# Performance work log

Hardware: AMD Instinct MI355X
Metric: run time of the kernel (lower is better)

## Reference

```python
import jax, jax.numpy as jnp
import numpy as np
import math

B, T, C = 2, 2048, 1024
H = 16            # n_head
RATIO = 4         # ratio_kv
HKV = H // RATIO  # n_head_kv = 4
HD = C // H       # head_dim = 64
G = H // HKV      # query heads per kv head = 4


def _alibi_slopes(n_heads):
    # n_heads must be a power of 2 here (H=16)
    assert math.log2(n_heads).is_integer()
    start = 2.0 ** (-(2.0 ** (-(math.log2(n_heads) - 3))))
    return np.array([start * (start ** i) for i in range(n_heads)], dtype=np.float32)


def setup_inputs() -> dict:
    key = jax.random.key(0)
    ks = jax.random.split(key, 5)
    return {
        "x": jax.random.normal(ks[0], (B, T, C), dtype=jnp.float32),
        "Wq": jax.random.normal(ks[1], (C, C), dtype=jnp.float32) * 0.02,
        "Wk": jax.random.normal(ks[2], (C, HKV * HD), dtype=jnp.float32) * 0.02,
        "Wv": jax.random.normal(ks[3], (C, HKV * HD), dtype=jnp.float32) * 0.02,
        "Wo": jax.random.normal(ks[4], (C, C), dtype=jnp.float32) * 0.02,
    }


def reference(x, Wq, Wk, Wv, Wo):
    # GQA causal attention with ALiBi bias (flash-disabled fallback path).
    # q: [B,HKV,G,T,HD] (grouped query heads), k/v: [B,HKV,T,HD]
    q = (x @ Wq).reshape(B, T, H, HD).transpose(0, 2, 1, 3).reshape(B, HKV, G, T, HD)
    k = (x @ Wk).reshape(B, T, HKV, HD).transpose(0, 2, 1, 3)
    v = (x @ Wv).reshape(B, T, HKV, HD).transpose(0, 2, 1, 3)

    scale = 1.0 / math.sqrt(HD)
    att = jnp.einsum('bkgtd,bksd->bkgts', q, k) * scale  # [B,HKV,G,T,T]

    # ALiBi: original repeats alibi(n_head) by G and truncates to n_head,
    # so query head h uses slope get_slopes(H)[h // G] == slopes[:HKV] per kv group.
    slopes = jnp.asarray(_alibi_slopes(H))[:HKV]          # [HKV]
    pos = jnp.arange(T)
    rel = (pos[None, :] - pos[:, None]).astype(jnp.float32)  # [T,T], rel[i,j]=j-i
    bias = slopes[:, None, None] * rel                    # [HKV,T,T]
    causal = jnp.triu(jnp.full((T, T), -jnp.inf, dtype=jnp.float32), 1)

    att = att + bias[None, :, None] + causal
    att = jax.nn.softmax(att.astype(jnp.float32), axis=-1).astype(q.dtype)

    y = jnp.einsum('bkgts,bksd->bkgtd', att, v)           # [B,HKV,G,T,HD]
    y = y.reshape(B, H, T, HD).transpose(0, 2, 1, 3).reshape(B, T, C)
    return y @ Wo
```

## Files before the change

kernel.cpp:

```cpp
#include <hip/hip_runtime.h>
#include <hip/hip_bf16.h>
#include <math.h>

#define B_ 2
#define T_ 2048
#define C_ 1024
#define H_ 16
#define HKV_ 4
#define G_ 4
#define HD_ 64
#define KVC_ 256
#define NQKV_ 1536
#define NQT_ 32

typedef __attribute__((ext_vector_type(8))) short bf16x8;
typedef __attribute__((ext_vector_type(4))) float f32x4;

static __device__ inline short f2bf(float f) {
    __hip_bfloat16 h = __float2bfloat16(f);
    short s;
    __builtin_memcpy(&s, &h, 2);
    return s;
}
static __device__ inline float bf2f(short s) {
    unsigned int u = ((unsigned int)(unsigned short)s) << 16;
    float f;
    __builtin_memcpy(&f, &u, 4);
    return f;
}

static __device__ inline void gload_lds16(const short* g, short* lds) {
    __builtin_amdgcn_global_load_lds(
        (const __attribute__((address_space(1))) unsigned int*)g,
        (__attribute__((address_space(3))) unsigned int*)lds, 16, 0, 0);
}

template <int CTRL>
static __device__ inline float dpp_mov(float x) {
    int xi = __builtin_bit_cast(int, x);
    int r = __builtin_amdgcn_update_dpp(0, xi, CTRL, 0xF, 0xF, true);
    return __builtin_bit_cast(float, r);
}
static __device__ inline float dpp_sum16(float x) {
    x += dpp_mov<0xB1>(x);
    x += dpp_mov<0x4E>(x);
    x += dpp_mov<0x141>(x);
    x += dpp_mov<0x140>(x);
    return x;
}

__global__ __launch_bounds__(256) void cast_bf16(
    const float* __restrict__ in, short* __restrict__ out, int n)
{
    const int i = (blockIdx.x * 256 + threadIdx.x) * 8;
    if (i >= n) return;
    const float4 a = *(const float4*)(in + i);
    const float4 b = *(const float4*)(in + i + 4);
    bf16x8 o;
    o[0] = f2bf(a.x); o[1] = f2bf(a.y); o[2] = f2bf(a.z); o[3] = f2bf(a.w);
    o[4] = f2bf(b.x); o[5] = f2bf(b.y); o[6] = f2bf(b.z); o[7] = f2bf(b.w);
    *(bf16x8*)(out + i) = o;
}

__global__ __launch_bounds__(256) void w_transpose(
    const float* __restrict__ Wq, const float* __restrict__ Wk,
    const float* __restrict__ Wv, const float* __restrict__ Wo,
    short* __restrict__ Wt, short* __restrict__ Wot)
{
    const int z = blockIdx.z;
    const float* in;
    short* out;
    int N;
    if (z == 0)      { in = Wq; out = Wt;                     N = C_; }
    else if (z == 1) { in = Wk; out = Wt + C_ * C_;           N = KVC_; }
    else if (z == 2) { in = Wv; out = Wt + (C_ + KVC_) * C_;  N = KVC_; }
    else             { in = Wo; out = Wot;                    N = C_; }
    const int n0 = blockIdx.x * 32;
    if (n0 >= N) return;
    __shared__ float t[32][33];
    const int tx = threadIdx.x, ty = threadIdx.y;
    const int k0 = blockIdx.y * 32;
    #pragma unroll
    for (int j = 0; j < 4; j++)
        t[ty + j * 8][tx] = in[(size_t)(k0 + ty + j * 8) * N + n0 + tx];
    __syncthreads();
    #pragma unroll
    for (int j = 0; j < 4; j++)
        out[(size_t)(n0 + ty + j * 8) * C_ + k0 + tx] = f2bf(t[tx][ty + j * 8]);
}

template <bool OUT_BF16>
__global__ __launch_bounds__(256) void gemm_bf16(
    const short* __restrict__ A, const short* __restrict__ Bt,
    void* __restrict__ Cout, int M, int N, int K)
{
    __shared__ short As[64 * 32];
    __shared__ short Bs[128 * 32];
    const int tid = threadIdx.x;
    const int wave = tid >> 6, lane = tid & 63;
    const int l15 = lane & 15, quad = lane >> 4;
    const int row0 = blockIdx.y * 64, col0 = blockIdx.x * 128;
    const int wrow = (wave >> 1) * 32, wcol = (wave & 1) * 64;

    f32x4 acc[2][4];
    #pragma unroll
    for (int i = 0; i < 2; i++)
        #pragma unroll
        for (int j = 0; j < 4; j++)
            acc[i][j] = (f32x4){0.f, 0.f, 0.f, 0.f};

    for (int kt = 0; kt < K; kt += 32) {
        __syncthreads();
        {
            const int r = wave * 16 + (lane >> 2);
            const int kof = (lane & 3) * 8;
            gload_lds16(A + (size_t)(row0 + r) * K + kt + kof, &As[wave * 512]);
        }
        #pragma unroll
        for (int c2 = 0; c2 < 2; c2++) {
            const int c = wave * 2 + c2;
            const int r = c * 16 + (lane >> 2);
            const int kof = (lane & 3) * 8;
            gload_lds16(Bt + (size_t)(col0 + r) * K + kt + kof, &Bs[c * 512]);
        }
        __syncthreads();

        bf16x8 af[2], bf[4];
        #pragma unroll
        for (int mt = 0; mt < 2; mt++)
            af[mt] = *(const bf16x8*)&As[(wrow + mt * 16 + l15) * 32 + quad * 8];
        #pragma unroll
        for (int nt = 0; nt < 4; nt++)
            bf[nt] = *(const bf16x8*)&Bs[(wcol + nt * 16 + l15) * 32 + quad * 8];
        #pragma unroll
        for (int mt = 0; mt < 2; mt++)
            #pragma unroll
            for (int nt = 0; nt < 4; nt++)
                acc[mt][nt] = __builtin_amdgcn_mfma_f32_16x16x32_bf16(
                    af[mt], bf[nt], acc[mt][nt], 0, 0, 0);
    }

    #pragma unroll
    for (int mt = 0; mt < 2; mt++) {
        #pragma unroll
        for (int r = 0; r < 4; r++) {
            const size_t row = row0 + wrow + mt * 16 + quad * 4 + r;
            #pragma unroll
            for (int nt = 0; nt < 4; nt++) {
                const size_t col = col0 + wcol + nt * 16 + l15;
                if (OUT_BF16)
                    ((short*)Cout)[row * N + col] = f2bf(acc[mt][nt][r]);
                else
                    ((float*)Cout)[row * N + col] = acc[mt][nt][r];
            }
        }
    }
}

__global__ __launch_bounds__(256) void kv_tile(
    const short* __restrict__ QKV, short* __restrict__ Kt, short* __restrict__ Vt)
{
    __shared__ short Ls[64 * 72];
    const int jt = blockIdx.x;
    const int bk = blockIdx.y;
    const int b = bk >> 2, kh = bk & 3;
    const int tid = threadIdx.x;
    const int key = tid >> 2, d16 = (tid & 3) * 16;
    const size_t src = (size_t)(b * T_ + jt * 64 + key) * NQKV_ + C_ + kh * 64 + d16;
    const size_t tbase = (size_t)(bk * 32 + jt) * 4096;

    {
        const int db0 = (tid & 3) * 2, db1 = db0 + 1;
        *(bf16x8*)(Kt + tbase + key * 64 + ((db0 ^ (key & 7)) * 8)) =
            *(const bf16x8*)(QKV + src);
        *(bf16x8*)(Kt + tbase + key * 64 + ((db1 ^ (key & 7)) * 8)) =
            *(const bf16x8*)(QKV + src + 8);
    }
    *(bf16x8*)&Ls[key * 72 + d16]     = *(const bf16x8*)(QKV + src + KVC_);
    *(bf16x8*)&Ls[key * 72 + d16 + 8] = *(const bf16x8*)(QKV + src + KVC_ + 8);
    __syncthreads();
    const int d = tid >> 2, k16 = (tid & 3) * 16;
    bf16x8 o0, o1;
    #pragma unroll
    for (int i = 0; i < 8; i++) o0[i] = Ls[(k16 + i) * 72 + d];
    #pragma unroll
    for (int i = 0; i < 8; i++) o1[i] = Ls[(k16 + 8 + i) * 72 + d];
    const int kb0 = (tid & 3) * 2, kb1 = kb0 + 1;
    *(bf16x8*)(Vt + tbase + d * 64 + ((kb0 ^ (d & 7)) * 8)) = o0;
    *(bf16x8*)(Vt + tbase + d * 64 + ((kb1 ^ (d & 7)) * 8)) = o1;
}

#define LSTR 72

__global__ __launch_bounds__(256) void attn_mfma(
    const short* __restrict__ QKV, const short* __restrict__ Ktg,
    const short* __restrict__ Vtg, short* __restrict__ Y)
{
    const int qx = blockIdx.x;
    const int bh = blockIdx.y;
    const int qtL = qx, qtH = NQT_ - 1 - qx;
    const int b = bh >> 4, h = bh & 15, kh = h >> 2;
    const float slope = exp2f(-0.5f * (float)(kh + 1));
    const int tid = threadIdx.x;
    const int wave = tid >> 6, lane = tid & 63;
    const int l15 = lane & 15, quad = lane >> 4;
    const int lswz = (l15 & 7) * 8;

    __shared__ short Ks[4096];
    __shared__ short Vs[4096];
    __shared__ short Ps[4 * 32 * LSTR];
    short* Pw = &Ps[wave * 32 * LSTR];
    const int wswz = ((quad >> 1) & 1) << 4;
    const int rswz = ((l15 >> 3) & 1) << 4;

    const size_t bT = (size_t)b * T_;
    const size_t tb0 = (size_t)((b * HKV_ + kh) * 32) * 4096;
    const int qrow0H = qtH * 64 + wave * 16;
    const int qrow0L = qtL * 64 + wave * 16;

    bf16x8 qfH[2], qfL[2];
    #pragma unroll
    for (int k0 = 0; k0 < 2; k0++) {
        const short* qpH = QKV + (bT + qrow0H + l15) * NQKV_ + h * 64;
        const short* qpL = QKV + (bT + qrow0L + l15) * NQKV_ + h * 64;
        bf16x8 rH = *(const bf16x8*)(qpH + k0 * 32 + quad * 8);
        bf16x8 rL = *(const bf16x8*)(qpL + k0 * 32 + quad * 8);
        #pragma unroll
        for (int j = 0; j < 8; j++) {
            qfH[k0][j] = f2bf(bf2f(rH[j]) * 0.125f);
            qfL[k0][j] = f2bf(bf2f(rL[j]) * 0.125f);
        }
    }

    f32x4 OaccH[4], OaccL[4];
    float psumH[4], psumL[4];
    #pragma unroll
    for (int nt = 0; nt < 4; nt++) {
        OaccH[nt] = (f32x4){0.f, 0.f, 0.f, 0.f};
        OaccL[nt] = (f32x4){0.f, 0.f, 0.f, 0.f};
    }
    #pragma unroll
    for (int r = 0; r < 4; r++) { psumH[r] = 0.f; psumL[r] = 0.f; }

    for (int jtk = 0; jtk <= qtH; jtk++) {
        __syncthreads();
        {
            const short* Ktile = Ktg + tb0 + (size_t)jtk * 4096;
            const short* Vtile = Vtg + tb0 + (size_t)jtk * 4096;
            #pragma unroll
            for (int i = 0; i < 2; i++) {
                const int ch = wave * 2 + i;
                gload_lds16(Ktile + ch * 512 + lane * 8, &Ks[ch * 512]);
                gload_lds16(Vtile + ch * 512 + lane * 8, &Vs[ch * 512]);
            }
        }
        __syncthreads();

        const bool doL = (jtk <= qtL);

        bf16x8 kf[8];
        #pragma unroll
        for (int nt = 0; nt < 4; nt++)
            #pragma unroll
            for (int k0 = 0; k0 < 2; k0++)
                kf[nt * 2 + k0] = *(const bf16x8*)
                    &Ks[(nt * 16 + l15) * 64 + (((k0 * 4 + quad) * 8) ^ lswz)];

        f32x4 sH[4], sL[4];
        #pragma unroll
        for (int nt = 0; nt < 4; nt++) {
            f32x4 a = {0.f, 0.f, 0.f, 0.f};
            a = __builtin_amdgcn_mfma_f32_16x16x32_bf16(qfH[0], kf[nt*2+0], a, 0, 0, 0);
            a = __builtin_amdgcn_mfma_f32_16x16x32_bf16(qfH[1], kf[nt*2+1], a, 0, 0, 0);
            sH[nt] = a;
        }
        if (doL) {
            #pragma unroll
            for (int nt = 0; nt < 4; nt++) {
                f32x4 a = {0.f, 0.f, 0.f, 0.f};
                a = __builtin_amdgcn_mfma_f32_16x16x32_bf16(qfL[0], kf[nt*2+0], a, 0, 0, 0);
                a = __builtin_amdgcn_mfma_f32_16x16x32_bf16(qfL[1], kf[nt*2+1], a, 0, 0, 0);
                sL[nt] = a;
            }
        }

        {
            const float relfH = (float)(jtk * 64 + l15 - quad * 4 - qrow0H);
            const bool mH = (jtk == qtH);
            #pragma unroll
            for (int nt = 0; nt < 4; nt++) {
                const int colsw = ((nt * 16 + l15) ^ wswz);
                #pragma unroll
                for (int r = 0; r < 4; r++) {
                    const float relv = relfH + (float)(nt * 16 - r);
                    float p = __expf(fmaf(slope, relv, sH[nt][r]));
                    if (mH && relv > 0.f) p = 0.f;
                    psumH[r] += p;
                    Pw[(quad * 4 + r) * LSTR + colsw] = f2bf(p);
                }
            }
        }
        if (doL) {
            const float relfL = (float)(jtk * 64 + l15 - quad * 4 - qrow0L);
            const bool mL = (jtk == qtL);
            #pragma unroll
            for (int nt = 0; nt < 4; nt++) {
                const int colsw = ((nt * 16 + l15) ^ wswz);
                #pragma unroll
                for (int r = 0; r < 4; r++) {
                    const float relv = relfL + (float)(nt * 16 - r);
                    float p = __expf(fmaf(slope, relv, sL[nt][r]));
                    if (mL && relv > 0.f) p = 0.f;
                    psumL[r] += p;
                    Pw[(16 + quad * 4 + r) * LSTR + colsw] = f2bf(p);
                }
            }
        }
        __asm__ volatile("s_waitcnt lgkmcnt(0)" ::: "memory");

        bf16x8 vf[8];
        #pragma unroll
        for (int nt = 0; nt < 4; nt++)
            #pragma unroll
            for (int k0 = 0; k0 < 2; k0++)
                vf[nt * 2 + k0] = *(const bf16x8*)
                    &Vs[(nt * 16 + l15) * 64 + (((k0 * 4 + quad) * 8) ^ lswz)];

        {
            bf16x8 pf0 = *(const bf16x8*)&Pw[l15 * LSTR + ((quad * 8) ^ rswz)];
            bf16x8 pf1 = *(const bf16x8*)&Pw[l15 * LSTR + ((32 + quad * 8) ^ rswz)];
            #pragma unroll
            for (int nt = 0; nt < 4; nt++) {
                OaccH[nt] = __builtin_amdgcn_mfma_f32_16x16x32_bf16(
                    pf0, vf[nt*2+0], OaccH[nt], 0, 0, 0);
                OaccH[nt] = __builtin_amdgcn_mfma_f32_16x16x32_bf16(
                    pf1, vf[nt*2+1], OaccH[nt], 0, 0, 0);
            }
        }
        if (doL) {
            bf16x8 pf0 = *(const bf16x8*)&Pw[(16 + l15) * LSTR + ((quad * 8) ^ rswz)];
            bf16x8 pf1 = *(const bf16x8*)&Pw[(16 + l15) * LSTR + ((32 + quad * 8) ^ rswz)];
            #pragma unroll
            for (int nt = 0; nt < 4; nt++) {
                OaccL[nt] = __builtin_amdgcn_mfma_f32_16x16x32_bf16(
                    pf0, vf[nt*2+0], OaccL[nt], 0, 0, 0);
                OaccL[nt] = __builtin_amdgcn_mfma_f32_16x16x32_bf16(
                    pf1, vf[nt*2+1], OaccL[nt], 0, 0, 0);
            }
        }
    }

    #pragma unroll
    for (int r = 0; r < 4; r++) {
        const float invH = 1.f / dpp_sum16(psumH[r]);
        const float invL = 1.f / dpp_sum16(psumL[r]);
        const int rowH = qrow0H + quad * 4 + r;
        const int rowL = qrow0L + quad * 4 + r;
        short* ypH = Y + (bT + rowH) * C_ + h * 64 + l15;
        short* ypL = Y + (bT + rowL) * C_ + h * 64 + l15;
        #pragma unroll
        for (int nt = 0; nt < 4; nt++) {
            ypH[nt * 16] = f2bf(OaccH[nt][r] * invH);
            ypL[nt * 16] = f2bf(OaccL[nt][r] * invL);
        }
    }
}

extern "C" void kernel_launch(void* const* d_in, const int* in_sizes, int n_in,
                              void* d_out, int out_size, void* d_ws, size_t ws_size,
                              hipStream_t stream) {
    const float* x  = (const float*)d_in[0];
    const float* Wq = (const float*)d_in[1];
    const float* Wk = (const float*)d_in[2];
    const float* Wv = (const float*)d_in[3];
    const float* Wo = (const float*)d_in[4];
    float* out = (float*)d_out;

    const int M = B_ * T_;
    short* xb  = (short*)d_ws;
    short* Wt  = xb  + (size_t)M * C_;
    short* Wot = Wt  + (size_t)NQKV_ * C_;
    short* QKV = Wot + (size_t)C_ * C_;
    short* Yb  = QKV + (size_t)M * NQKV_;
    short* Ktg = Yb  + (size_t)M * C_;
    short* Vtg = Ktg + (size_t)8 * 32 * 4096;

    cast_bf16<<<dim3(M * C_ / (256 * 8)), dim3(256), 0, stream>>>(x, xb, M * C_);
    w_transpose<<<dim3(32, 32, 4), dim3(32, 8), 0, stream>>>(Wq, Wk, Wv, Wo, Wt, Wot);

    gemm_bf16<true><<<dim3(NQKV_ / 128, M / 64), dim3(256), 0, stream>>>(
        xb, Wt, QKV, M, NQKV_, C_);
    kv_tile<<<dim3(32, 8), dim3(256), 0, stream>>>(QKV, Ktg, Vtg);
    attn_mfma<<<dim3(NQT_ / 2, B_ * H_), dim3(256), 0, stream>>>(QKV, Ktg, Vtg, Yb);
    gemm_bf16<false><<<dim3(C_ / 128, M / 64), dim3(256), 0, stream>>>(
        Yb, Wot, out, M, C_, C_);
}
```

Before: 182.2 us.

## Compute softmax row sums via MFMA with ones and use exp2 with truncated bf16

Folds log2(e) into the query scale and ALiBi slope so the exponent becomes a raw exp2, and splits the diagonal tile from the others so only the last tile pays for the causal mask check. The per-lane psum accumulation and final DPP reduction are replaced by extra MFMAs of P against a ones vector, so the row sums come from the same bf16 P values used for P·V. P is converted to bf16 by truncation instead of rounding, which makes the VALU-heavy softmax section cheaper. In exchange it adds two MFMAs per tile per half and introduces a slight downward bias in P from truncation.

```diff
diff --git a/kernel.cpp b/kernel.cpp
--- a/kernel.cpp
+++ b/kernel.cpp
@@ -22,6 +22,11 @@
     __builtin_memcpy(&s, &h, 2);
     return s;
 }
+static __device__ inline short f2bf_trunc(float f) {
+    unsigned int u;
+    __builtin_memcpy(&u, &f, 4);
+    return (short)(u >> 16);
+}
 static __device__ inline float bf2f(short s) {
     unsigned int u = ((unsigned int)(unsigned short)s) << 16;
     float f;
@@ -33,20 +38,6 @@
     __builtin_amdgcn_global_load_lds(
         (const __attribute__((address_space(1))) unsigned int*)g,
         (__attribute__((address_space(3))) unsigned int*)lds, 16, 0, 0);
-}
-
-template <int CTRL>
-static __device__ inline float dpp_mov(float x) {
-    int xi = __builtin_bit_cast(int, x);
-    int r = __builtin_amdgcn_update_dpp(0, xi, CTRL, 0xF, 0xF, true);
-    return __builtin_bit_cast(float, r);
-}
-static __device__ inline float dpp_sum16(float x) {
-    x += dpp_mov<0xB1>(x);
-    x += dpp_mov<0x4E>(x);
-    x += dpp_mov<0x141>(x);
-    x += dpp_mov<0x140>(x);
-    return x;
 }
 
 __global__ __launch_bounds__(256) void cast_bf16(
@@ -200,7 +191,7 @@
     const int bh = blockIdx.y;
     const int qtL = qx, qtH = NQT_ - 1 - qx;
     const int b = bh >> 4, h = bh & 15, kh = h >> 2;
-    const float slope = exp2f(-0.5f * (float)(kh + 1));
+    const float slope2 = exp2f(-0.5f * (float)(kh + 1)) * 1.44269504f;
     const int tid = threadIdx.x;
     const int wave = tid >> 6, lane = tid & 63;
     const int l15 = lane & 15, quad = lane >> 4;
@@ -218,6 +209,7 @@
     const int qrow0H = qtH * 64 + wave * 16;
     const int qrow0L = qtL * 64 + wave * 16;
 
+    const float qscale = 0.125f * 1.44269504f;
     bf16x8 qfH[2], qfL[2];
     #pragma unroll
     for (int k0 = 0; k0 < 2; k0++) {
@@ -227,20 +219,22 @@
         bf16x8 rL = *(const bf16x8*)(qpL + k0 * 32 + quad * 8);
         #pragma unroll
         for (int j = 0; j < 8; j++) {
-            qfH[k0][j] = f2bf(bf2f(rH[j]) * 0.125f);
-            qfL[k0][j] = f2bf(bf2f(rL[j]) * 0.125f);
-        }
-    }
-
-    f32x4 OaccH[4], OaccL[4];
-    float psumH[4], psumL[4];
+            qfH[k0][j] = f2bf(bf2f(rH[j]) * qscale);
+            qfL[k0][j] = f2bf(bf2f(rL[j]) * qscale);
+        }
+    }
+
+    const short one_s = (short)0x3F80;
+    const bf16x8 ones = {one_s, one_s, one_s, one_s, one_s, one_s, one_s, one_s};
+
+    f32x4 OaccH[4], OaccL[4], laccH, laccL;
     #pragma unroll
     for (int nt = 0; nt < 4; nt++) {
         OaccH[nt] = (f32x4){0.f, 0.f, 0.f, 0.f};
         OaccL[nt] = (f32x4){0.f, 0.f, 0.f, 0.f};
     }
-    #pragma unroll
-    for (int r = 0; r < 4; r++) { psumH[r] = 0.f; psumL[r] = 0.f; }
+    laccH = (f32x4){0.f, 0.f, 0.f, 0.f};
+    laccL = (f32x4){0.f, 0.f, 0.f, 0.f};
 
     for (int jtk = 0; jtk <= qtH; jtk++) {
         __syncthreads();
@@ -285,34 +279,60 @@
         }
 
         {
-            const float relfH = (float)(jtk * 64 + l15 - quad * 4 - qrow0H);
-            const bool mH = (jtk == qtH);
-            #pragma unroll
-            for (int nt = 0; nt < 4; nt++) {
-                const int colsw = ((nt * 16 + l15) ^ wswz);
+            const float base = slope2 * (float)(jtk * 64 + l15 - quad * 4 - qrow0H);
+            if (jtk == qtH) {
                 #pragma unroll
-                for (int r = 0; r < 4; r++) {
-                    const float relv = relfH + (float)(nt * 16 - r);
-                    float p = __expf(fmaf(slope, relv, sH[nt][r]));
-                    if (mH && relv > 0.f) p = 0.f;
-                    psumH[r] += p;
-                    Pw[(quad * 4 + r) * LSTR + colsw] = f2bf(p);
+                for (int nt = 0; nt < 4; nt++) {
+                    const int colsw = ((nt * 16 + l15) ^ wswz);
+                    #pragma unroll
+                    for (int r = 0; r < 4; r++) {
+                        const float relv = (float)(jtk * 64 + l15 - quad * 4 - qrow0H)
+                                         + (float)(nt * 16 - r);
+                        float p = __builtin_amdgcn_exp2f(
+                            fmaf(slope2, (float)(nt * 16 - r), base) + sH[nt][r]);
+                        if (relv > 0.f) p = 0.f;
+                        Pw[(quad * 4 + r) * LSTR + colsw] = f2bf_trunc(p);
+                    }
                 }
+            } else {
+                #pragma unroll
+                for (int nt = 0; nt < 4; nt++) {
+                    const int colsw = ((nt * 16 + l15) ^ wswz);
+                    #pragma unroll
+                    for (int r = 0; r < 4; r++) {
+                        float p = __builtin_amdgcn_exp2f(
+                            fmaf(slope2, (float)(nt * 16 - r), base) + sH[nt][r]);
+                        Pw[(quad * 4 + r) * LSTR + colsw] = f2bf_trunc(p);
+                    }
+                }
             }
         }
         if (doL) {
-            const float relfL = (float)(jtk * 64 + l15 - quad * 4 - qrow0L);
-            const bool mL = (jtk == qtL);
-            #pragma unroll
-            for (int nt = 0; nt < 4; nt++) {
-                const int colsw = ((nt * 16 + l15) ^ wswz);
+            const float base = slope2 * (float)(jtk * 64 + l15 - quad * 4 - qrow0L);
+            if (jtk == qtL) {
                 #pragma unroll
-                for (int r = 0; r < 4; r++) {
-                    const float relv = relfL + (float)(nt * 16 - r);
-                    float p = __expf(fmaf(slope, relv, sL[nt][r]));
-                    if (mL && relv > 0.f) p = 0.f;
-                    psumL[r] += p;
-                    Pw[(16 + quad * 4 + r) * LSTR + colsw] = f2bf(p);
+                for (int nt = 0; nt < 4; nt++) {
+                    const int colsw = ((nt * 16 + l15) ^ wswz);
+                    #pragma unroll
+                    for (int r = 0; r < 4; r++) {
+                        const float relv = (float)(jtk * 64 + l15 - quad * 4 - qrow0L)
+                                         + (float)(nt * 16 - r);
+                        float p = __builtin_amdgcn_exp2f(
+                            fmaf(slope2, (float)(nt * 16 - r), base) + sL[nt][r]);
+                        if (relv > 0.f) p = 0.f;
+                        Pw[(16 + quad * 4 + r) * LSTR + colsw] = f2bf_trunc(p);
+                    }
+                }
+            } else {
+                #pragma unroll
+                for (int nt = 0; nt < 4; nt++) {
+                    const int colsw = ((nt * 16 + l15) ^ wswz);
+                    #pragma unroll
+                    for (int r = 0; r < 4; r++) {
+                        float p = __builtin_amdgcn_exp2f(
+                            fmaf(slope2, (float)(nt * 16 - r), base) + sL[nt][r]);
+                        Pw[(16 + quad * 4 + r) * LSTR + colsw] = f2bf_trunc(p);
+                    }
                 }
             }
         }
@@ -329,6 +349,8 @@
         {
             bf16x8 pf0 = *(const bf16x8*)&Pw[l15 * LSTR + ((quad * 8) ^ rswz)];
             bf16x8 pf1 = *(const bf16x8*)&Pw[l15 * LSTR + ((32 + quad * 8) ^ rswz)];
+            laccH = __builtin_amdgcn_mfma_f32_16x16x32_bf16(pf0, ones, laccH, 0, 0, 0);
+            laccH = __builtin_amdgcn_mfma_f32_16x16x32_bf16(pf1, ones, laccH, 0, 0, 0);
             #pragma unroll
             for (int nt = 0; nt < 4; nt++) {
                 OaccH[nt] = __builtin_amdgcn_mfma_f32_16x16x32_bf16(
@@ -340,6 +362,8 @@
         if (doL) {
             bf16x8 pf0 = *(const bf16x8*)&Pw[(16 + l15) * LSTR + ((quad * 8) ^ rswz)];
             bf16x8 pf1 = *(const bf16x8*)&Pw[(16 + l15) * LSTR + ((32 + quad * 8) ^ rswz)];
+            laccL = __builtin_amdgcn_mfma_f32_16x16x32_bf16(pf0, ones, laccL, 0, 0, 0);
+            laccL = __builtin_amdgcn_mfma_f32_16x16x32_bf16(pf1, ones, laccL, 0, 0, 0);
             #pragma unroll
             for (int nt = 0; nt < 4; nt++) {
                 OaccL[nt] = __builtin_amdgcn_mfma_f32_16x16x32_bf16(
@@ -352,8 +376,8 @@
 
     #pragma unroll
     for (int r = 0; r < 4; r++) {
-        const float invH = 1.f / dpp_sum16(psumH[r]);
-        const float invL = 1.f / dpp_sum16(psumL[r]);
+        const float invH = 1.f / laccH[r];
+        const float invL = 1.f / laccL[r];
         const int rowH = qrow0H + quad * 4 + r;
         const int rowL = qrow0L + quad * 4 + r;
         short* ypH = Y + (bT + rowH) * C_ + h * 64 + l15;
```

Result: faster. 176.1 us (-3.3%).
